# Performance work log

Hardware: AMD Instinct MI355X
Metric: run time of the kernel (lower is better)

The kernel has to match this reference:

```python
import jax, jax.numpy as jnp
import numpy as np

N = 8192
IN_DIM = 512
OUT_DIM = 256
ALPHA = 0.2  # LeakyReLU negative slope


def setup_inputs() -> dict:
    key = jax.random.key(0)
    k_nodes, k_edge, k_W, k_Wb, k_a1, k_a1b, k_a2, k_a2b = jax.random.split(key, 8)
    nodes = jax.random.normal(k_nodes, (N, IN_DIM), dtype=jnp.float32)
    edge_mat = jax.random.uniform(k_edge, (N, N)) > 0.5
    edge_mat = edge_mat | jnp.eye(N, dtype=bool)
    s_W = 1.0 / np.sqrt(IN_DIM)
    s_a = 1.0 / np.sqrt(OUT_DIM)
    W_w = jax.random.uniform(k_W, (OUT_DIM, IN_DIM), minval=-s_W, maxval=s_W, dtype=jnp.float32)
    W_b = jax.random.uniform(k_Wb, (OUT_DIM,), minval=-s_W, maxval=s_W, dtype=jnp.float32)
    a1_w = jax.random.uniform(k_a1, (1, OUT_DIM), minval=-s_a, maxval=s_a, dtype=jnp.float32)
    a1_b = jax.random.uniform(k_a1b, (1,), minval=-s_a, maxval=s_a, dtype=jnp.float32)
    a2_w = jax.random.uniform(k_a2, (1, OUT_DIM), minval=-s_a, maxval=s_a, dtype=jnp.float32)
    a2_b = jax.random.uniform(k_a2b, (1,), minval=-s_a, maxval=s_a, dtype=jnp.float32)
    return {"nodes": nodes, "edge_mat": edge_mat, "W_w": W_w, "W_b": W_b,
            "a1_w": a1_w, "a1_b": a1_b, "a2_w": a2_w, "a2_b": a2_b}


def reference(nodes, edge_mat, W_w, W_b, a1_w, a1_b, a2_w, a2_b):
    Wh = nodes @ W_w.T + W_b                      # [N, OUT_DIM]
    Wh1 = Wh @ a1_w.T + a1_b                      # [N, 1]
    Wh2 = Wh @ a2_w.T + a2_b                      # [N, 1]
    scores = jax.nn.leaky_relu(Wh1 + Wh2.T, negative_slope=ALPHA)  # [N, N]
    masked = jnp.where(edge_mat, scores, -jnp.inf)
    attention = jax.nn.softmax(masked, axis=1)    # [N, N]
    return attention @ Wh                         # [N, OUT_DIM]
```

## Files before the change

### kernel.cpp

```cpp
#include <hip/hip_runtime.h>
#include <hip/hip_bf16.h>
#include <stdint.h>


#define NN 8192
#define IND 512
#define OUTD 256

typedef __attribute__((ext_vector_type(8))) short short8;
typedef __attribute__((ext_vector_type(4))) short short4v;
typedef __attribute__((ext_vector_type(4))) float f32x4;
typedef __attribute__((ext_vector_type(4))) unsigned int u32x4;

#define AS_GLOBAL __attribute__((address_space(1)))
#define AS_LDS __attribute__((address_space(3)))

static __device__ __forceinline__ short f2bf(float f) {
  return __builtin_bit_cast(short, __float2bfloat16(f));
}

extern "C" __global__ __launch_bounds__(256) void k_convert_w(
    const float* __restrict__ W, short* __restrict__ W2) {
  const int t = blockIdx.x * 256 + threadIdx.x;
  const int row = t >> 6, kb = t & 63;
  const float* src = W + row * IND + kb * 8;
  f32x4 x0 = *(const f32x4*)src;
  f32x4 x1 = *(const f32x4*)(src + 4);
  short8 o;
  o[0] = f2bf(x0[0]); o[1] = f2bf(x0[1]); o[2] = f2bf(x0[2]); o[3] = f2bf(x0[3]);
  o[4] = f2bf(x1[0]); o[5] = f2bf(x1[1]); o[6] = f2bf(x1[2]); o[7] = f2bf(x1[3]);
  *(short8*)(W2 + (size_t)kb * 2048 + row * 8) = o;
}

extern "C" __global__ __launch_bounds__(128) void k_wh(
    const float* __restrict__ nodes, const short* __restrict__ W2,
    const float* __restrict__ Wb, const float* __restrict__ a1w,
    const float* __restrict__ a1b, const float* __restrict__ a2w,
    const float* __restrict__ a2b, short* __restrict__ WhL,
    float* __restrict__ s1, float* __restrict__ s2) {
  const int tid = threadIdx.x;
  const int wv = tid >> 6, lane = tid & 63, g = lane >> 4, m = lane & 15;
  const int rowbase = blockIdx.x * 32 + wv * 16;

  f32x4 acc[16];
#pragma unroll
  for (int nf = 0; nf < 16; ++nf) acc[nf] = (f32x4){0.f, 0.f, 0.f, 0.f};

  const float* arow = nodes + (size_t)(rowbase + m) * IND;
  const short* bb = W2 + (size_t)g * 2048 + m * 8;
#pragma unroll 4
  for (int k0 = 0; k0 < IND; k0 += 32) {
    const float* ap = arow + k0 + g * 8;
    f32x4 x0 = *(const f32x4*)ap;
    f32x4 x1 = *(const f32x4*)(ap + 4);
    short8 af;
    af[0] = f2bf(x0[0]); af[1] = f2bf(x0[1]); af[2] = f2bf(x0[2]); af[3] = f2bf(x0[3]);
    af[4] = f2bf(x1[0]); af[5] = f2bf(x1[1]); af[6] = f2bf(x1[2]); af[7] = f2bf(x1[3]);
    const short* bk = bb + (size_t)(k0 >> 3) * 2048;
#pragma unroll
    for (int nf = 0; nf < 16; ++nf) {
      short8 bf = *(const short8*)(bk + nf * 128);
      acc[nf] = __builtin_amdgcn_mfma_f32_16x16x32_bf16(af, bf, acc[nf], 0, 0, 0);
    }
  }

  float p1[4] = {0.f, 0.f, 0.f, 0.f}, p2[4] = {0.f, 0.f, 0.f, 0.f};
#pragma unroll
  for (int nf = 0; nf < 16; ++nf) {
    const int n = nf * 16 + m;
    const float b = Wb[n], c1 = a1w[n], c2 = a2w[n];
#pragma unroll
    for (int r = 0; r < 4; ++r) {
      float v = acc[nf][r] + b;
      acc[nf][r] = v;
      p1[r] += c1 * v;
      p2[r] += c2 * v;
    }
  }
#pragma unroll
  for (int off = 1; off < 16; off <<= 1) {
#pragma unroll
    for (int r = 0; r < 4; ++r) {
      p1[r] += __shfl_xor(p1[r], off);
      p2[r] += __shfl_xor(p2[r], off);
    }
  }
  if (m == 0) {
    const float b1 = a1b[0], b2 = a2b[0];
#pragma unroll
    for (int r = 0; r < 4; ++r) {
      const int row = rowbase + g * 4 + r;
      s1[row] = p1[r] + b1;
      s2[row] = p2[r] + b2;
    }
  }

  const size_t cbase = ((size_t)(rowbase >> 3) + (g >> 1)) * 2048 + (g & 1) * 4;
#pragma unroll
  for (int nf = 0; nf < 16; ++nf) {
    short4v o;
#pragma unroll
    for (int r = 0; r < 4; ++r) o[r] = f2bf(acc[nf][r]);
    *(short4v*)(WhL + cbase + (size_t)(nf * 16 + m) * 8) = o;
  }
}

extern "C" __global__ __launch_bounds__(256) void k_prep(
    const float* __restrict__ s1, const float* __restrict__ s2,
    float* __restrict__ sAC, uint32_t* __restrict__ sPK) {
  const int i = blockIdx.x * 256 + threadIdx.x;
  const float v1 = s1[i], v2 = s2[i];
  sAC[i] = __expf(v1);
  sAC[NN + i] = __expf(0.2f * v1);
  const float B = __expf(v2), D = __expf(0.2f * v2);
  sPK[2 * i] = __builtin_bit_cast(uint32_t, B);
  sPK[2 * i + 1] =
      ((uint32_t)(uint16_t)f2bf(D) << 16) | (uint16_t)(uint16_t)f2bf(v2);
}

extern "C" __global__ __launch_bounds__(256) void k_mask(
    const int* __restrict__ mask, uint32_t* __restrict__ bm) {
  const int tid = threadIdx.x;
  const int wv = tid >> 6, lane = tid & 63;
  const int gw = blockIdx.x * 4 + wv;
  const size_t base = (size_t)gw * 16384;
#pragma unroll 4
  for (int it = 0; it < 64; ++it) {
    const size_t ib = base + (size_t)it * 256;
    unsigned long long b0 = __ballot(mask[ib + lane] != 0);
    unsigned long long b1 = __ballot(mask[ib + 64 + lane] != 0);
    unsigned long long b2 = __ballot(mask[ib + 128 + lane] != 0);
    unsigned long long b3 = __ballot(mask[ib + 192 + lane] != 0);
    if (lane < 8) {
      unsigned long long s01 = (lane & 2) ? b1 : b0;
      unsigned long long s23 = (lane & 2) ? b3 : b2;
      unsigned long long sel = (lane & 4) ? s23 : s01;
      bm[ib / 32 + lane] = (uint32_t)(sel >> ((lane & 1) * 32));
    }
  }
}

extern "C" __global__ __launch_bounds__(256, 4) void k_attn(
    const uint32_t* __restrict__ bm, const short* __restrict__ WhL,
    const float* __restrict__ s1, const float* __restrict__ sAC,
    const uint32_t* __restrict__ sPK,
    float* __restrict__ pnum, float* __restrict__ pden) {
  __shared__ short Bs[2][8192];
  __shared__ uint32_t PKs[2048];

  const int tid = threadIdx.x;
  const int w = tid >> 6, lane = tid & 63, g = lane >> 4, m = lane & 15;
  const int rt = blockIdx.x >> 3, jc = blockIdx.x & 7;
  const int rg = w & 1, ns = w >> 1;
  const int rb = rt * 64 + rg * 32;

  const float T0 = -s1[rb + m],        T1 = -s1[rb + 16 + m];
  const float A0 = sAC[rb + m],        A1 = sAC[rb + 16 + m];
  const float C0 = sAC[NN + rb + m],   C1 = sAC[NN + rb + 16 + m];

  f32x4 acc0[8], acc1[8];
#pragma unroll
  for (int nf = 0; nf < 8; ++nf) {
    acc0[nf] = (f32x4){0.f, 0.f, 0.f, 0.f};
    acc1[nf] = (f32x4){0.f, 0.f, 0.f, 0.f};
  }
  float den0 = 0.f, den1 = 0.f;

  const uint32_t* bw0 = bm + (size_t)(rb + m) * 256 + jc * 32;
  const uint32_t* bw1 = bw0 + (size_t)16 * 256;
  const short* gWu = WhL + (size_t)jc * 262144 + w * 2048 + lane * 8;

#pragma unroll
  for (int c = 0; c < 2; ++c) {
    __builtin_amdgcn_global_load_lds(
        (const AS_GLOBAL void*)((const char*)sPK + (size_t)jc * 8192 +
                                w * 2048 + c * 1024 + lane * 16),
        (AS_LDS void*)((char*)PKs + w * 2048 + c * 1024), 16, 0, 0);
  }
#pragma unroll
  for (int c = 0; c < 4; ++c) {
    __builtin_amdgcn_global_load_lds(
        (const AS_GLOBAL void*)(gWu + c * 512),
        (AS_LDS void*)(&Bs[0][w * 2048 + c * 512]), 16, 0, 0);
  }
  uint32_t cw0 = bw0[0], cw1 = bw1[0];
  __syncthreads();

  auto build = [&](float T, float A, float C, uint32_t mbits,
                   const u32x4& q0, const u32x4& q1,
                   const u32x4& q2, const u32x4& q3, float& den) -> short8 {
    const uint32_t Bv[8] = {q0[0], q0[2], q1[0], q1[2],
                            q2[0], q2[2], q3[0], q3[2]};
    const uint32_t Dv[8] = {q0[1], q0[3], q1[1], q1[3],
                            q2[1], q2[3], q3[1], q3[3]};
    short8 af;
#pragma unroll
    for (int i = 0; i < 8; ++i) {
      const float s2v = __builtin_bit_cast(float, Dv[i] << 16);
      const bool pos = s2v > T;
      const float wv = __builtin_bit_cast(float, pos ? Bv[i] : (Dv[i] & 0xFFFF0000u));
      const float a = pos ? A : C;
      const float val = wv * a;
      const float pv = ((mbits >> i) & 1u) ? val : 0.f;
      den += pv;
      af[i] = f2bf(pv);
    }
    return af;
  };

  for (int u = 0; u < 32; ++u) {
    if (u < 31) {
      const short* gn = gWu + (size_t)(u + 1) * 8192;
      short* ld = &Bs[(u + 1) & 1][w * 2048];
#pragma unroll
      for (int c = 0; c < 4; ++c) {
        __builtin_amdgcn_global_load_lds(
            (const AS_GLOBAL void*)(gn + c * 512),
            (AS_LDS void*)(ld + c * 512), 16, 0, 0);
      }
    }
    const int un = (u < 31) ? u + 1 : 31;
    const uint32_t nw0 = bw0[un], nw1 = bw1[un];

    const uint32_t* pk = &PKs[(u * 32 + g * 8) * 2];
    const u32x4 q0 = *(const u32x4*)(pk + 0);
    const u32x4 q1 = *(const u32x4*)(pk + 4);
    const u32x4 q2 = *(const u32x4*)(pk + 8);
    const u32x4 q3 = *(const u32x4*)(pk + 12);
    short8 af0 = build(T0, A0, C0, cw0 >> (g * 8), q0, q1, q2, q3, den0);
    short8 af1 = build(T1, A1, C1, cw1 >> (g * 8), q0, q1, q2, q3, den1);
    const short* bl = &Bs[u & 1][g * 2048 + (ns * 128 + m) * 8];
#pragma unroll
    for (int nf = 0; nf < 8; ++nf) {
      short8 bf = *(const short8*)(bl + nf * 128);
      acc0[nf] = __builtin_amdgcn_mfma_f32_16x16x32_bf16(af0, bf, acc0[nf], 0, 0, 0);
      acc1[nf] = __builtin_amdgcn_mfma_f32_16x16x32_bf16(af1, bf, acc1[nf], 0, 0, 0);
    }
    cw0 = nw0; cw1 = nw1;
    __syncthreads();
  }

  den0 += __shfl_xor(den0, 16); den0 += __shfl_xor(den0, 32);
  den1 += __shfl_xor(den1, 16); den1 += __shfl_xor(den1, 32);
  if (ns == 0 && lane < 16) {
    pden[jc * NN + rb + m] = den0;
    pden[jc * NN + rb + 16 + m] = den1;
  }

  float* pn = pnum + (size_t)jc * NN * OUTD + (size_t)rb * OUTD + ns * 128;
#pragma unroll
  for (int r = 0; r < 4; ++r) {
    const int q = g * 4 + r;
#pragma unroll
    for (int nf = 0; nf < 8; ++nf) {
      pn[(size_t)q * OUTD + nf * 16 + m] = acc0[nf][r];
      pn[(size_t)(16 + q) * OUTD + nf * 16 + m] = acc1[nf][r];
    }
  }
}

extern "C" __global__ __launch_bounds__(256) void k_comb(
    const float* __restrict__ pnum, const float* __restrict__ pden,
    float* __restrict__ out) {
  const int idx = blockIdx.x * 256 + threadIdx.x;
  const int row = idx >> 6, c4 = (idx & 63) * 4;
  f32x4 s = (f32x4){0.f, 0.f, 0.f, 0.f};
  float d = 0.f;
#pragma unroll
  for (int jc = 0; jc < 8; ++jc) {
    f32x4 v = *(const f32x4*)(pnum + ((size_t)jc * NN + row) * OUTD + c4);
    s += v;
    d += pden[jc * NN + row];
  }
  const float inv = 1.f / d;
  *(f32x4*)(out + (size_t)row * OUTD + c4) = s * inv;
}

extern "C" void kernel_launch(void* const* d_in, const int* in_sizes, int n_in,
                              void* d_out, int out_size, void* d_ws, size_t ws_size,
                              hipStream_t stream) {
  const float* nodes = (const float*)d_in[0];
  const int*   mask  = (const int*)d_in[1];
  const float* W_w   = (const float*)d_in[2];
  const float* W_b   = (const float*)d_in[3];
  const float* a1w   = (const float*)d_in[4];
  const float* a1b   = (const float*)d_in[5];
  const float* a2w   = (const float*)d_in[6];
  const float* a2b   = (const float*)d_in[7];
  float* out = (float*)d_out;

  char* ws = (char*)d_ws;
  short*    WhL  = (short*)(ws);
  float*    s1   = (float*)(ws + (size_t)4  * 1024 * 1024);
  float*    s2   = (float*)(ws + (size_t)4  * 1024 * 1024 + 32768);
  short*    W2   = (short*)(ws + (size_t)4  * 1024 * 1024 + 65536);
  uint32_t* bmp  = (uint32_t*)(ws + (size_t)5  * 1024 * 1024);
  float*    sAC  = (float*)(ws + (size_t)13 * 1024 * 1024);
  uint32_t* sPK  = (uint32_t*)(ws + (size_t)14 * 1024 * 1024);
  float*    pnum = (float*)(ws + (size_t)16 * 1024 * 1024);
  float*    pden = (float*)(ws + (size_t)96 * 1024 * 1024);

  hipLaunchKernelGGL(k_mask, dim3(1024), dim3(256), 0, stream, mask, bmp);
  hipLaunchKernelGGL(k_convert_w, dim3(64), dim3(256), 0, stream, W_w, W2);
  hipLaunchKernelGGL(k_wh, dim3(256), dim3(128), 0, stream,
                     nodes, W2, W_b, a1w, a1b, a2w, a2b, WhL, s1, s2);
  hipLaunchKernelGGL(k_prep, dim3(32), dim3(256), 0, stream, s1, s2, sAC, sPK);
  hipLaunchKernelGGL(k_attn, dim3(1024), dim3(256), 0, stream,
                     bmp, WhL, s1, sAC, sPK, pnum, pden);
  hipLaunchKernelGGL(k_comb, dim3(2048), dim3(256), 0, stream,
                     pnum, pden, out);
}
```

Baseline: 177.8 us.

## Enlarge attention block to 128 rows with triple-buffered LDS pipeline

```diff
diff --git a/kernel.cpp b/kernel.cpp
--- a/kernel.cpp
+++ b/kernel.cpp
@@ -140,19 +140,20 @@
   }
 }
 
-extern "C" __global__ __launch_bounds__(256, 4) void k_attn(
+extern "C" __global__ __launch_bounds__(512, 4) void k_attn(
     const uint32_t* __restrict__ bm, const short* __restrict__ WhL,
     const float* __restrict__ s1, const float* __restrict__ sAC,
     const uint32_t* __restrict__ sPK,
     float* __restrict__ pnum, float* __restrict__ pden) {
-  __shared__ short Bs[2][8192];
-  __shared__ uint32_t PKs[2048];
+  __shared__ char smem[73728];
+  uint32_t* PKs = (uint32_t*)(smem + 49152);
+  uint32_t* BMs = (uint32_t*)(smem + 57344);
 
   const int tid = threadIdx.x;
   const int w = tid >> 6, lane = tid & 63, g = lane >> 4, m = lane & 15;
   const int rt = blockIdx.x >> 3, jc = blockIdx.x & 7;
-  const int rg = w & 1, ns = w >> 1;
-  const int rb = rt * 64 + rg * 32;
+  const int rg = w & 3, ns = w >> 2;
+  const int rb = rt * 128 + rg * 32;
 
   const float T0 = -s1[rb + m],        T1 = -s1[rb + 16 + m];
   const float A0 = sAC[rb + m],        A1 = sAC[rb + 16 + m];
@@ -166,24 +167,32 @@
   }
   float den0 = 0.f, den1 = 0.f;
 
-  const uint32_t* bw0 = bm + (size_t)(rb + m) * 256 + jc * 32;
-  const uint32_t* bw1 = bw0 + (size_t)16 * 256;
-  const short* gWu = WhL + (size_t)jc * 262144 + w * 2048 + lane * 8;
-
-#pragma unroll
-  for (int c = 0; c < 2; ++c) {
-    __builtin_amdgcn_global_load_lds(
-        (const AS_GLOBAL void*)((const char*)sPK + (size_t)jc * 8192 +
-                                w * 2048 + c * 1024 + lane * 16),
-        (AS_LDS void*)((char*)PKs + w * 2048 + c * 1024), 16, 0, 0);
-  }
-#pragma unroll
-  for (int c = 0; c < 4; ++c) {
-    __builtin_amdgcn_global_load_lds(
-        (const AS_GLOBAL void*)(gWu + c * 512),
-        (AS_LDS void*)(&Bs[0][w * 2048 + c * 512]), 16, 0, 0);
-  }
-  uint32_t cw0 = bw0[0], cw1 = bw1[0];
+  {
+    const int rloc = tid >> 2, wq = (tid & 3) * 8;
+    const uint32_t* src = bm + (size_t)(rt * 128 + rloc) * 256 + jc * 32 + wq;
+    u32x4 a = *(const u32x4*)src;
+    u32x4 b = *(const u32x4*)(src + 4);
+#pragma unroll
+    for (int i = 0; i < 4; ++i)
+      BMs[rloc * 32 + ((wq + i) ^ (rloc & 31))] = a[i];
+#pragma unroll
+    for (int i = 0; i < 4; ++i)
+      BMs[rloc * 32 + ((wq + 4 + i) ^ (rloc & 31))] = b[i];
+  }
+  __builtin_amdgcn_global_load_lds(
+      (const AS_GLOBAL void*)((const char*)sPK + (size_t)jc * 8192 +
+                              w * 1024 + lane * 16),
+      (AS_LDS void*)(smem + 49152 + w * 1024), 16, 0, 0);
+  const short* gS = WhL + (size_t)jc * 262144;
+#pragma unroll
+  for (int s = 0; s < 2; ++s) {
+#pragma unroll
+    for (int c = 0; c < 2; ++c) {
+      __builtin_amdgcn_global_load_lds(
+          (const AS_GLOBAL void*)(gS + s * 8192 + w * 1024 + c * 512 + lane * 8),
+          (AS_LDS void*)(smem + s * 16384 + w * 2048 + c * 1024), 16, 0, 0);
+    }
+  }
   __syncthreads();
 
   auto build = [&](float T, float A, float C, uint32_t mbits,
@@ -209,35 +218,39 @@
   };
 
   for (int u = 0; u < 32; ++u) {
-    if (u < 31) {
-      const short* gn = gWu + (size_t)(u + 1) * 8192;
-      short* ld = &Bs[(u + 1) & 1][w * 2048];
-#pragma unroll
-      for (int c = 0; c < 4; ++c) {
-        __builtin_amdgcn_global_load_lds(
-            (const AS_GLOBAL void*)(gn + c * 512),
-            (AS_LDS void*)(ld + c * 512), 16, 0, 0);
-      }
-    }
-    const int un = (u < 31) ? u + 1 : 31;
-    const uint32_t nw0 = bw0[un], nw1 = bw1[un];
-
-    const uint32_t* pk = &PKs[(u * 32 + g * 8) * 2];
+    asm volatile("s_waitcnt vmcnt(2)" ::: "memory");
+    __builtin_amdgcn_s_barrier();
+    __builtin_amdgcn_sched_barrier(0);
+
+    {
+      const int up = (u + 2 < 32) ? (u + 2) : 31;
+      const int bi = (u + 2) % 3;
+      const short* gn = gS + up * 8192 + w * 1024 + lane * 8;
+      char* ldb = smem + bi * 16384 + w * 2048;
+      __builtin_amdgcn_global_load_lds((const AS_GLOBAL void*)gn,
+                                       (AS_LDS void*)ldb, 16, 0, 0);
+      __builtin_amdgcn_global_load_lds((const AS_GLOBAL void*)(gn + 512),
+                                       (AS_LDS void*)(ldb + 1024), 16, 0, 0);
+    }
+
+    const uint32_t cw0 = BMs[(rg * 32 + m) * 32 + (u ^ m)];
+    const uint32_t cw1 = BMs[(rg * 32 + 16 + m) * 32 + (u ^ (16 + m))];
+    const uint32_t* pk = &PKs[u * 64 + g * 16];
     const u32x4 q0 = *(const u32x4*)(pk + 0);
     const u32x4 q1 = *(const u32x4*)(pk + 4);
     const u32x4 q2 = *(const u32x4*)(pk + 8);
     const u32x4 q3 = *(const u32x4*)(pk + 12);
     short8 af0 = build(T0, A0, C0, cw0 >> (g * 8), q0, q1, q2, q3, den0);
     short8 af1 = build(T1, A1, C1, cw1 >> (g * 8), q0, q1, q2, q3, den1);
-    const short* bl = &Bs[u & 1][g * 2048 + (ns * 128 + m) * 8];
+
+    const short* bl = (const short*)(smem + (u % 3) * 16384) +
+                      g * 2048 + (ns * 128 + m) * 8;
 #pragma unroll
     for (int nf = 0; nf < 8; ++nf) {
       short8 bf = *(const short8*)(bl + nf * 128);
       acc0[nf] = __builtin_amdgcn_mfma_f32_16x16x32_bf16(af0, bf, acc0[nf], 0, 0, 0);
       acc1[nf] = __builtin_amdgcn_mfma_f32_16x16x32_bf16(af1, bf, acc1[nf], 0, 0, 0);
     }
-    cw0 = nw0; cw1 = nw1;
-    __syncthreads();
   }
 
   den0 += __shfl_xor(den0, 16); den0 += __shfl_xor(den0, 32);
@@ -305,7 +318,7 @@
   hipLaunchKernelGGL(k_wh, dim3(256), dim3(128), 0, stream,
                      nodes, W2, W_b, a1w, a1b, a2w, a2b, WhL, s1, s2);
   hipLaunchKernelGGL(k_prep, dim3(32), dim3(256), 0, stream, s1, s2, sAC, sPK);
-  hipLaunchKernelGGL(k_attn, dim3(1024), dim3(256), 0, stream,
+  hipLaunchKernelGGL(k_attn, dim3(512), dim3(512), 0, stream,
                      bmp, WhL, s1, sAC, sPK, pnum, pden);
   hipLaunchKernelGGL(k_comb, dim3(2048), dim3(256), 0, stream,
                      pnum, pden, out);
```

Measured after the change: 175.4 us. No clear change (-1.3%).

## Fuse mask bit-packing into attention kernel by reading int mask directly

Applied to the files above, without the earlier changes.

```diff
diff --git a/kernel.cpp b/kernel.cpp
--- a/kernel.cpp
+++ b/kernel.cpp
@@ -10,6 +10,7 @@
 typedef __attribute__((ext_vector_type(8))) short short8;
 typedef __attribute__((ext_vector_type(4))) short short4v;
 typedef __attribute__((ext_vector_type(4))) float f32x4;
+typedef __attribute__((ext_vector_type(4))) int i32x4;
 typedef __attribute__((ext_vector_type(4))) unsigned int u32x4;
 
 #define AS_GLOBAL __attribute__((address_space(1)))
@@ -118,30 +119,8 @@
       ((uint32_t)(uint16_t)f2bf(D) << 16) | (uint16_t)(uint16_t)f2bf(v2);
 }
 
-extern "C" __global__ __launch_bounds__(256) void k_mask(
-    const int* __restrict__ mask, uint32_t* __restrict__ bm) {
-  const int tid = threadIdx.x;
-  const int wv = tid >> 6, lane = tid & 63;
-  const int gw = blockIdx.x * 4 + wv;
-  const size_t base = (size_t)gw * 16384;
-#pragma unroll 4
-  for (int it = 0; it < 64; ++it) {
-    const size_t ib = base + (size_t)it * 256;
-    unsigned long long b0 = __ballot(mask[ib + lane] != 0);
-    unsigned long long b1 = __ballot(mask[ib + 64 + lane] != 0);
-    unsigned long long b2 = __ballot(mask[ib + 128 + lane] != 0);
-    unsigned long long b3 = __ballot(mask[ib + 192 + lane] != 0);
-    if (lane < 8) {
-      unsigned long long s01 = (lane & 2) ? b1 : b0;
-      unsigned long long s23 = (lane & 2) ? b3 : b2;
-      unsigned long long sel = (lane & 4) ? s23 : s01;
-      bm[ib / 32 + lane] = (uint32_t)(sel >> ((lane & 1) * 32));
-    }
-  }
-}
-
 extern "C" __global__ __launch_bounds__(256, 4) void k_attn(
-    const uint32_t* __restrict__ bm, const short* __restrict__ WhL,
+    const int* __restrict__ mask, const short* __restrict__ WhL,
     const float* __restrict__ s1, const float* __restrict__ sAC,
     const uint32_t* __restrict__ sPK,
     float* __restrict__ pnum, float* __restrict__ pden) {
@@ -166,8 +145,8 @@
   }
   float den0 = 0.f, den1 = 0.f;
 
-  const uint32_t* bw0 = bm + (size_t)(rb + m) * 256 + jc * 32;
-  const uint32_t* bw1 = bw0 + (size_t)16 * 256;
+  const int* mr0 = mask + (size_t)(rb + m) * NN + jc * 1024 + g * 8;
+  const int* mr1 = mr0 + (size_t)16 * NN;
   const short* gWu = WhL + (size_t)jc * 262144 + w * 2048 + lane * 8;
 
 #pragma unroll
@@ -183,10 +162,13 @@
         (const AS_GLOBAL void*)(gWu + c * 512),
         (AS_LDS void*)(&Bs[0][w * 2048 + c * 512]), 16, 0, 0);
   }
-  uint32_t cw0 = bw0[0], cw1 = bw1[0];
+  i32x4 cm0a = __builtin_nontemporal_load((const i32x4*)mr0);
+  i32x4 cm0b = __builtin_nontemporal_load((const i32x4*)(mr0 + 4));
+  i32x4 cm1a = __builtin_nontemporal_load((const i32x4*)mr1);
+  i32x4 cm1b = __builtin_nontemporal_load((const i32x4*)(mr1 + 4));
   __syncthreads();
 
-  auto build = [&](float T, float A, float C, uint32_t mbits,
+  auto build = [&](float T, float A, float C, const i32x4& lo, const i32x4& hi,
                    const u32x4& q0, const u32x4& q1,
                    const u32x4& q2, const u32x4& q3, float& den) -> short8 {
     const uint32_t Bv[8] = {q0[0], q0[2], q1[0], q1[2],
@@ -201,7 +183,8 @@
       const float wv = __builtin_bit_cast(float, pos ? Bv[i] : (Dv[i] & 0xFFFF0000u));
       const float a = pos ? A : C;
       const float val = wv * a;
-      const float pv = ((mbits >> i) & 1u) ? val : 0.f;
+      const int mv = (i < 4) ? lo[i] : hi[i - 4];
+      const float pv = (mv != 0) ? val : 0.f;
       den += pv;
       af[i] = f2bf(pv);
     }
@@ -220,15 +203,18 @@
       }
     }
     const int un = (u < 31) ? u + 1 : 31;
-    const uint32_t nw0 = bw0[un], nw1 = bw1[un];
+    i32x4 nm0a = __builtin_nontemporal_load((const i32x4*)(mr0 + un * 32));
+    i32x4 nm0b = __builtin_nontemporal_load((const i32x4*)(mr0 + un * 32 + 4));
+    i32x4 nm1a = __builtin_nontemporal_load((const i32x4*)(mr1 + un * 32));
+    i32x4 nm1b = __builtin_nontemporal_load((const i32x4*)(mr1 + un * 32 + 4));
 
     const uint32_t* pk = &PKs[(u * 32 + g * 8) * 2];
     const u32x4 q0 = *(const u32x4*)(pk + 0);
     const u32x4 q1 = *(const u32x4*)(pk + 4);
     const u32x4 q2 = *(const u32x4*)(pk + 8);
     const u32x4 q3 = *(const u32x4*)(pk + 12);
-    short8 af0 = build(T0, A0, C0, cw0 >> (g * 8), q0, q1, q2, q3, den0);
-    short8 af1 = build(T1, A1, C1, cw1 >> (g * 8), q0, q1, q2, q3, den1);
+    short8 af0 = build(T0, A0, C0, cm0a, cm0b, q0, q1, q2, q3, den0);
+    short8 af1 = build(T1, A1, C1, cm1a, cm1b, q0, q1, q2, q3, den1);
     const short* bl = &Bs[u & 1][g * 2048 + (ns * 128 + m) * 8];
 #pragma unroll
     for (int nf = 0; nf < 8; ++nf) {
@@ -236,7 +222,7 @@
       acc0[nf] = __builtin_amdgcn_mfma_f32_16x16x32_bf16(af0, bf, acc0[nf], 0, 0, 0);
       acc1[nf] = __builtin_amdgcn_mfma_f32_16x16x32_bf16(af1, bf, acc1[nf], 0, 0, 0);
     }
-    cw0 = nw0; cw1 = nw1;
+    cm0a = nm0a; cm0b = nm0b; cm1a = nm1a; cm1b = nm1b;
     __syncthreads();
   }
 
@@ -294,19 +280,17 @@
   float*    s1   = (float*)(ws + (size_t)4  * 1024 * 1024);
   float*    s2   = (float*)(ws + (size_t)4  * 1024 * 1024 + 32768);
   short*    W2   = (short*)(ws + (size_t)4  * 1024 * 1024 + 65536);
-  uint32_t* bmp  = (uint32_t*)(ws + (size_t)5  * 1024 * 1024);
   float*    sAC  = (float*)(ws + (size_t)13 * 1024 * 1024);
   uint32_t* sPK  = (uint32_t*)(ws + (size_t)14 * 1024 * 1024);
   float*    pnum = (float*)(ws + (size_t)16 * 1024 * 1024);
   float*    pden = (float*)(ws + (size_t)96 * 1024 * 1024);
 
-  hipLaunchKernelGGL(k_mask, dim3(1024), dim3(256), 0, stream, mask, bmp);
   hipLaunchKernelGGL(k_convert_w, dim3(64), dim3(256), 0, stream, W_w, W2);
   hipLaunchKernelGGL(k_wh, dim3(256), dim3(128), 0, stream,
                      nodes, W2, W_b, a1w, a1b, a2w, a2b, WhL, s1, s2);
   hipLaunchKernelGGL(k_prep, dim3(32), dim3(256), 0, stream, s1, s2, sAC, sPK);
   hipLaunchKernelGGL(k_attn, dim3(1024), dim3(256), 0, stream,
-                     bmp, WhL, s1, sAC, sPK, pnum, pden);
+                     mask, WhL, s1, sAC, sPK, pnum, pden);
   hipLaunchKernelGGL(k_comb, dim3(2048), dim3(256), 0, stream,
                      pnum, pden, out);
 }
```

Result: slower. 201.7 us (+13.4%).

## Fuse prep into Wh kernel and enlarge attention tiles to 128 rows

Applied to the files above, without the earlier changes.

```diff
diff --git a/kernel.cpp b/kernel.cpp
--- a/kernel.cpp
+++ b/kernel.cpp
@@ -37,7 +37,8 @@
     const float* __restrict__ Wb, const float* __restrict__ a1w,
     const float* __restrict__ a1b, const float* __restrict__ a2w,
     const float* __restrict__ a2b, short* __restrict__ WhL,
-    float* __restrict__ s1, float* __restrict__ s2) {
+    float* __restrict__ s1, float* __restrict__ sAC,
+    uint32_t* __restrict__ sPK) {
   const int tid = threadIdx.x;
   const int wv = tid >> 6, lane = tid & 63, g = lane >> 4, m = lane & 15;
   const int rowbase = blockIdx.x * 32 + wv * 16;
@@ -90,8 +91,14 @@
 #pragma unroll
     for (int r = 0; r < 4; ++r) {
       const int row = rowbase + g * 4 + r;
-      s1[row] = p1[r] + b1;
-      s2[row] = p2[r] + b2;
+      const float v1 = p1[r] + b1, v2 = p2[r] + b2;
+      s1[row] = v1;
+      sAC[row] = __expf(v1);
+      sAC[NN + row] = __expf(0.2f * v1);
+      const float B = __expf(v2), D = __expf(0.2f * v2);
+      sPK[2 * row] = __builtin_bit_cast(uint32_t, B);
+      sPK[2 * row + 1] =
+          ((uint32_t)(uint16_t)f2bf(D) << 16) | (uint16_t)f2bf(v2);
     }
   }
 
@@ -103,19 +110,6 @@
     for (int r = 0; r < 4; ++r) o[r] = f2bf(acc[nf][r]);
     *(short4v*)(WhL + cbase + (size_t)(nf * 16 + m) * 8) = o;
   }
-}
-
-extern "C" __global__ __launch_bounds__(256) void k_prep(
-    const float* __restrict__ s1, const float* __restrict__ s2,
-    float* __restrict__ sAC, uint32_t* __restrict__ sPK) {
-  const int i = blockIdx.x * 256 + threadIdx.x;
-  const float v1 = s1[i], v2 = s2[i];
-  sAC[i] = __expf(v1);
-  sAC[NN + i] = __expf(0.2f * v1);
-  const float B = __expf(v2), D = __expf(0.2f * v2);
-  sPK[2 * i] = __builtin_bit_cast(uint32_t, B);
-  sPK[2 * i + 1] =
-      ((uint32_t)(uint16_t)f2bf(D) << 16) | (uint16_t)(uint16_t)f2bf(v2);
 }
 
 extern "C" __global__ __launch_bounds__(256) void k_mask(
@@ -140,19 +134,19 @@
   }
 }
 
-extern "C" __global__ __launch_bounds__(256, 4) void k_attn(
+extern "C" __global__ __launch_bounds__(512, 4) void k_attn(
     const uint32_t* __restrict__ bm, const short* __restrict__ WhL,
     const float* __restrict__ s1, const float* __restrict__ sAC,
     const uint32_t* __restrict__ sPK,
     float* __restrict__ pnum, float* __restrict__ pden) {
-  __shared__ short Bs[2][8192];
-  __shared__ uint32_t PKs[2048];
+  __shared__ char smem[73728];
+  uint32_t* PKs = (uint32_t*)(smem + 65536);
 
   const int tid = threadIdx.x;
   const int w = tid >> 6, lane = tid & 63, g = lane >> 4, m = lane & 15;
   const int rt = blockIdx.x >> 3, jc = blockIdx.x & 7;
-  const int rg = w & 1, ns = w >> 1;
-  const int rb = rt * 64 + rg * 32;
+  const int rg = w & 3, ns = w >> 2;
+  const int rb = rt * 128 + rg * 32;
 
   const float T0 = -s1[rb + m],        T1 = -s1[rb + 16 + m];
   const float A0 = sAC[rb + m],        A1 = sAC[rb + 16 + m];
@@ -168,22 +162,20 @@
 
   const uint32_t* bw0 = bm + (size_t)(rb + m) * 256 + jc * 32;
   const uint32_t* bw1 = bw0 + (size_t)16 * 256;
-  const short* gWu = WhL + (size_t)jc * 262144 + w * 2048 + lane * 8;
-
-#pragma unroll
-  for (int c = 0; c < 2; ++c) {
-    __builtin_amdgcn_global_load_lds(
-        (const AS_GLOBAL void*)((const char*)sPK + (size_t)jc * 8192 +
-                                w * 2048 + c * 1024 + lane * 16),
-        (AS_LDS void*)((char*)PKs + w * 2048 + c * 1024), 16, 0, 0);
-  }
+  const short* gS = WhL + (size_t)jc * 262144;
+
+  __builtin_amdgcn_global_load_lds(
+      (const AS_GLOBAL void*)((const char*)sPK + (size_t)jc * 8192 +
+                              w * 1024 + lane * 16),
+      (AS_LDS void*)(smem + 65536 + w * 1024), 16, 0, 0);
 #pragma unroll
   for (int c = 0; c < 4; ++c) {
     __builtin_amdgcn_global_load_lds(
-        (const AS_GLOBAL void*)(gWu + c * 512),
-        (AS_LDS void*)(&Bs[0][w * 2048 + c * 512]), 16, 0, 0);
-  }
-  uint32_t cw0 = bw0[0], cw1 = bw1[0];
+        (const AS_GLOBAL void*)(gS + w * 2048 + c * 512 + lane * 8),
+        (AS_LDS void*)(smem + w * 4096 + c * 1024), 16, 0, 0);
+  }
+  uint64_t cw0 = *(const uint64_t*)(bw0);
+  uint64_t cw1 = *(const uint64_t*)(bw1);
   __syncthreads();
 
   auto build = [&](float T, float A, float C, uint32_t mbits,
@@ -208,33 +200,43 @@
     return af;
   };
 
-  for (int u = 0; u < 32; ++u) {
-    if (u < 31) {
-      const short* gn = gWu + (size_t)(u + 1) * 8192;
-      short* ld = &Bs[(u + 1) & 1][w * 2048];
+  for (int u = 0; u < 16; ++u) {
+    if (u < 15) {
+      const short* gn = gS + (u + 1) * 16384 + w * 2048 + lane * 8;
+      char* ld = smem + ((u + 1) & 1) * 32768 + w * 4096;
 #pragma unroll
       for (int c = 0; c < 4; ++c) {
         __builtin_amdgcn_global_load_lds(
             (const AS_GLOBAL void*)(gn + c * 512),
-            (AS_LDS void*)(ld + c * 512), 16, 0, 0);
+            (AS_LDS void*)(ld + c * 1024), 16, 0, 0);
       }
     }
-    const int un = (u < 31) ? u + 1 : 31;
-    const uint32_t nw0 = bw0[un], nw1 = bw1[un];
-
-    const uint32_t* pk = &PKs[(u * 32 + g * 8) * 2];
-    const u32x4 q0 = *(const u32x4*)(pk + 0);
-    const u32x4 q1 = *(const u32x4*)(pk + 4);
-    const u32x4 q2 = *(const u32x4*)(pk + 8);
-    const u32x4 q3 = *(const u32x4*)(pk + 12);
-    short8 af0 = build(T0, A0, C0, cw0 >> (g * 8), q0, q1, q2, q3, den0);
-    short8 af1 = build(T1, A1, C1, cw1 >> (g * 8), q0, q1, q2, q3, den1);
-    const short* bl = &Bs[u & 1][g * 2048 + (ns * 128 + m) * 8];
-#pragma unroll
-    for (int nf = 0; nf < 8; ++nf) {
-      short8 bf = *(const short8*)(bl + nf * 128);
-      acc0[nf] = __builtin_amdgcn_mfma_f32_16x16x32_bf16(af0, bf, acc0[nf], 0, 0, 0);
-      acc1[nf] = __builtin_amdgcn_mfma_f32_16x16x32_bf16(af1, bf, acc1[nf], 0, 0, 0);
+    const int un = (u < 15) ? u + 1 : 15;
+    const uint64_t nw0 = *(const uint64_t*)(bw0 + 2 * un);
+    const uint64_t nw1 = *(const uint64_t*)(bw1 + 2 * un);
+
+    const char* bufb = smem + (u & 1) * 32768;
+#pragma unroll
+    for (int h = 0; h < 2; ++h) {
+      const uint32_t* pk = &PKs[u * 128 + h * 64 + g * 16];
+      const u32x4 q0 = *(const u32x4*)(pk + 0);
+      const u32x4 q1 = *(const u32x4*)(pk + 4);
+      const u32x4 q2 = *(const u32x4*)(pk + 8);
+      const u32x4 q3 = *(const u32x4*)(pk + 12);
+      const uint32_t mb0 = (uint32_t)(cw0 >> (h * 32)) >> (g * 8);
+      const uint32_t mb1 = (uint32_t)(cw1 >> (h * 32)) >> (g * 8);
+      short8 af0 = build(T0, A0, C0, mb0, q0, q1, q2, q3, den0);
+      short8 af1 = build(T1, A1, C1, mb1, q0, q1, q2, q3, den1);
+      const short* bl = (const short*)bufb + (h * 4 + g) * 2048 +
+                        (ns * 128 + m) * 8;
+      __builtin_amdgcn_s_setprio(1);
+#pragma unroll
+      for (int nf = 0; nf < 8; ++nf) {
+        short8 bf = *(const short8*)(bl + nf * 128);
+        acc0[nf] = __builtin_amdgcn_mfma_f32_16x16x32_bf16(af0, bf, acc0[nf], 0, 0, 0);
+        acc1[nf] = __builtin_amdgcn_mfma_f32_16x16x32_bf16(af1, bf, acc1[nf], 0, 0, 0);
+      }
+      __builtin_amdgcn_s_setprio(0);
     }
     cw0 = nw0; cw1 = nw1;
     __syncthreads();
@@ -292,7 +294,6 @@
   char* ws = (char*)d_ws;
   short*    WhL  = (short*)(ws);
   float*    s1   = (float*)(ws + (size_t)4  * 1024 * 1024);
-  float*    s2   = (float*)(ws + (size_t)4  * 1024 * 1024 + 32768);
   short*    W2   = (short*)(ws + (size_t)4  * 1024 * 1024 + 65536);
   uint32_t* bmp  = (uint32_t*)(ws + (size_t)5  * 1024 * 1024);
   float*    sAC  = (float*)(ws + (size_t)13 * 1024 * 1024);
@@ -303,9 +304,8 @@
   hipLaunchKernelGGL(k_mask, dim3(1024), dim3(256), 0, stream, mask, bmp);
   hipLaunchKernelGGL(k_convert_w, dim3(64), dim3(256), 0, stream, W_w, W2);
   hipLaunchKernelGGL(k_wh, dim3(256), dim3(128), 0, stream,
-                     nodes, W2, W_b, a1w, a1b, a2w, a2b, WhL, s1, s2);
-  hipLaunchKernelGGL(k_prep, dim3(32), dim3(256), 0, stream, s1, s2, sAC, sPK);
-  hipLaunchKernelGGL(k_attn, dim3(1024), dim3(256), 0, stream,
+                     nodes, W2, W_b, a1w, a1b, a2w, a2b, WhL, s1, sAC, sPK);
+  hipLaunchKernelGGL(k_attn, dim3(512), dim3(512), 0, stream,
                      bmp, WhL, s1, sAC, sPK, pnum, pden);
   hipLaunchKernelGGL(k_comb, dim3(2048), dim3(256), 0, stream,
                      pnum, pden, out);
```

New measurement: 400.6 us. 2.25x slower.
